# Performance work log

Hardware: AMD Instinct MI355X
Metric: run time of the kernel (lower is better)

## Reference

```python
import jax, jax.numpy as jnp
import numpy as np

A, V, T = 32, 32, 128          # per-modality hidden dims
PF = 128                       # post_fusion_dim
FUSED = (A + 1) * (V + 1) * (T + 1)  # 140481
B = 256


def setup_inputs() -> dict:
    key = jax.random.key(0)
    ks = jax.random.split(key, 9)
    s1 = 1.0 / np.sqrt(FUSED)
    s2 = 1.0 / np.sqrt(PF)
    return {
        "audio_x": jax.random.normal(ks[0], (B, A), dtype=jnp.float32),
        "video_x": jax.random.normal(ks[1], (B, V), dtype=jnp.float32),
        "text_x": jax.random.normal(ks[2], (B, T), dtype=jnp.float32),
        "W1": jax.random.uniform(ks[3], (FUSED, PF), jnp.float32, -s1, s1),
        "b1": jax.random.uniform(ks[4], (PF,), jnp.float32, -s1, s1),
        "W2": jax.random.uniform(ks[5], (PF, PF), jnp.float32, -s2, s2),
        "b2": jax.random.uniform(ks[6], (PF,), jnp.float32, -s2, s2),
        "W3": jax.random.uniform(ks[7], (PF, 1), jnp.float32, -s2, s2),
        "b3": jax.random.uniform(ks[8], (1,), jnp.float32, -s2, s2),
    }


def reference(audio_x, video_x, text_x, W1, b1, W2, b2, W3, b3):
    b = audio_x.shape[0]
    ones = jnp.ones((b, 1), dtype=audio_x.dtype)
    a = jnp.concatenate([ones, audio_x], axis=1)  # (B, A+1)
    v = jnp.concatenate([ones, video_x], axis=1)  # (B, V+1)
    t = jnp.concatenate([ones, text_x], axis=1)   # (B, T+1)
    # trilinear outer product, flattened: (B, (A+1)*(V+1)*(T+1))
    fusion = jnp.einsum("ba,bv,bt->bavt", a, v, t).reshape(b, -1)
    h1 = jax.nn.relu(fusion @ W1 + b1)
    h2 = jax.nn.relu(h1 @ W2 + b2)
    return h2 @ W3 + b3
```

## Files before the change

kernel.cpp:

```cpp
#include <hip/hip_runtime.h>
#include <hip/hip_bf16.h>
#include <stdint.h>

#define BATCH 256
#define PFD 128
#define T1 129
#define NPAIRS 1089
#define BK2 136
#define CHUNK 8

typedef short bf16x8 __attribute__((ext_vector_type(8)));
typedef float f32x4 __attribute__((ext_vector_type(4)));

static __device__ __forceinline__ float float_of(unsigned u){ union{float f;unsigned u;}x;x.u=u;return x.f; }
static __device__ __forceinline__ unsigned pk_bf16(float a, float b){
  union { __hip_bfloat162 h; unsigned u; } c;
  c.h = __float22bfloat162_rn(make_float2(a, b));
  return c.u;
}

__global__ __launch_bounds__(512, 2) void tfn_k1(
    const float* __restrict__ audio, const float* __restrict__ video,
    const float* __restrict__ text, const float* __restrict__ W1,
    unsigned short* __restrict__ part, int S) {
  __shared__ __align__(16) short b_lds[2][PFD * BK2];
  __shared__ __align__(16) float av_lds[BATCH * CHUNK];

  const int tid = threadIdx.x;
  const int bk = blockIdx.x;
  const int npb = NPAIRS / S, rem0 = NPAIRS % S;
  const int p0 = bk * npb + (bk < rem0 ? bk : rem0);
  const int np = npb + (bk < rem0 ? 1 : 0);

  const int wave = tid >> 6, lane = tid & 63;
  const int l15 = lane & 15, quad = lane >> 4;
  const int sn = tid & 127, skg = tid >> 7;

  float treg[2][32];
  float t128r[2];
  #pragma unroll
  for (int mt = 0; mt < 2; ++mt) {
    const int m = wave * 32 + mt * 16 + l15;
    t128r[mt] = text[m * 128 + 127];
    #pragma unroll
    for (int ks = 0; ks < 4; ++ks)
      #pragma unroll
      for (int j = 0; j < 8; ++j) {
        const int it = ks * 32 + quad * 8 + j;
        treg[mt][ks * 8 + j] = (it == 0) ? 1.0f : text[m * 128 + it - 1];
      }
  }

  f32x4 acc[2][8];
  #pragma unroll
  for (int a = 0; a < 2; ++a)
    #pragma unroll
    for (int b = 0; b < 8; ++b) acc[a][b] = f32x4{0.f, 0.f, 0.f, 0.f};

  float pf[32], rv[8];

  for (int c0 = 0; c0 < np; c0 += CHUNK) {
    const int nc = (np - c0) < CHUNK ? (np - c0) : CHUNK;
    const int pbase = p0 + c0;
    __syncthreads();
    if (tid < BATCH) {
      const int m = tid;
      for (int j = 0; j < nc; ++j) {
        int p = pbase + j;
        int ia = p / 33, iv = p - ia * 33;
        float a = (ia == 0) ? 1.0f : audio[m * 32 + ia - 1];
        float v = (iv == 0) ? 1.0f : video[m * 32 + iv - 1];
        av_lds[m * CHUNK + j] = a * v;
      }
    }
    #pragma unroll
    for (int j = 0; j < 8; ++j) {
      int kk = skg * 8 + j;
      rv[j] = (kk < nc) ? W1[((long)(pbase + kk) * T1 + 128) * PFD + sn] : 0.0f;
    }
    {
      const long rb = (long)pbase * T1;
      #pragma unroll
      for (int g = 0; g < 4; ++g)
        #pragma unroll
        for (int j = 0; j < 8; ++j)
          pf[g * 8 + j] = W1[(rb + g * 32 + skg * 8 + j) * PFD + sn];
    }
    for (int sp = 0; sp < nc; ++sp) {
      {
        union { bf16x8 v; unsigned u[4]; } w;
        #pragma unroll
        for (int g = 0; g < 4; ++g) {
          #pragma unroll
          for (int d = 0; d < 4; ++d)
            w.u[d] = pk_bf16(pf[g * 8 + 2 * d], pf[g * 8 + 2 * d + 1]);
          *(bf16x8*)&b_lds[sp & 1][sn * BK2 + g * 32 + skg * 8] = w.v;
        }
      }
      __syncthreads();
      if (sp + 1 < nc) {
        const long rb = (long)(pbase + sp + 1) * T1;
        #pragma unroll
        for (int g = 0; g < 4; ++g)
          #pragma unroll
          for (int j = 0; j < 8; ++j)
            pf[g * 8 + j] = W1[(rb + g * 32 + skg * 8 + j) * PFD + sn];
      }
      const float avm0 = av_lds[(wave * 32 + l15) * CHUNK + sp];
      const float avm1 = av_lds[(wave * 32 + 16 + l15) * CHUNK + sp];
      #pragma unroll
      for (int ks = 0; ks < 4; ++ks) {
        bf16x8 A0, A1;
        {
          union { bf16x8 v; unsigned u[4]; } c0u, c1u;
          #pragma unroll
          for (int d = 0; d < 4; ++d) {
            c0u.u[d] = pk_bf16(avm0 * treg[0][ks * 8 + 2 * d], avm0 * treg[0][ks * 8 + 2 * d + 1]);
            c1u.u[d] = pk_bf16(avm1 * treg[1][ks * 8 + 2 * d], avm1 * treg[1][ks * 8 + 2 * d + 1]);
          }
          A0 = c0u.v; A1 = c1u.v;
        }
        #pragma unroll
        for (int nt = 0; nt < 8; ++nt) {
          bf16x8 bf = *(const bf16x8*)&b_lds[sp & 1][(nt * 16 + l15) * BK2 + ks * 32 + quad * 8];
          acc[0][nt] = __builtin_amdgcn_mfma_f32_16x16x32_bf16(A0, bf, acc[0][nt], 0, 0, 0);
          acc[1][nt] = __builtin_amdgcn_mfma_f32_16x16x32_bf16(A1, bf, acc[1][nt], 0, 0, 0);
        }
      }
    }
    __syncthreads();
    {
      union { bf16x8 v; unsigned u[4]; } w;
      #pragma unroll
      for (int d = 0; d < 4; ++d) w.u[d] = pk_bf16(rv[2 * d], rv[2 * d + 1]);
      *(bf16x8*)&b_lds[0][sn * BK2 + skg * 8] = w.v;
    }
    __syncthreads();
    {
      bf16x8 A[2];
      #pragma unroll
      for (int mt = 0; mt < 2; ++mt) {
        const int m = wave * 32 + mt * 16 + l15;
        union { bf16x8 v; unsigned u[4]; } c;
        #pragma unroll
        for (int d = 0; d < 4; ++d) {
          int k0 = quad * 8 + 2 * d, k1 = k0 + 1;
          float f0 = (k0 < nc) ? av_lds[m * CHUNK + k0] * t128r[mt] : 0.0f;
          float f1 = (k1 < nc) ? av_lds[m * CHUNK + k1] * t128r[mt] : 0.0f;
          c.u[d] = pk_bf16(f0, f1);
        }
        A[mt] = c.v;
      }
      #pragma unroll
      for (int nt = 0; nt < 8; ++nt) {
        bf16x8 bf = *(const bf16x8*)&b_lds[0][(nt * 16 + l15) * BK2 + quad * 8];
        acc[0][nt] = __builtin_amdgcn_mfma_f32_16x16x32_bf16(A[0], bf, acc[0][nt], 0, 0, 0);
        acc[1][nt] = __builtin_amdgcn_mfma_f32_16x16x32_bf16(A[1], bf, acc[1][nt], 0, 0, 0);
      }
    }
  }

  #pragma unroll
  for (int mt = 0; mt < 2; ++mt)
    #pragma unroll
    for (int r = 0; r < 4; ++r) {
      const int m = wave * 32 + mt * 16 + quad * 4 + r;
      union { bf16x8 v; unsigned u[4]; } w;
      #pragma unroll
      for (int d = 0; d < 4; ++d) w.u[d] = pk_bf16(acc[mt][2 * d][r], acc[mt][2 * d + 1][r]);
      *(bf16x8*)&part[((size_t)m * S + bk) * PFD + l15 * 8] = w.v;
    }
}

__global__ __launch_bounds__(1024) void tfn_k2(
    const unsigned short* __restrict__ part, const float* __restrict__ b1,
    const float* __restrict__ W2, const float* __restrict__ b2,
    const float* __restrict__ W3, const float* __restrict__ b3,
    float* __restrict__ out, int S) {
  __shared__ float sred[1024 * 4];
  __shared__ float h1s[PFD];
  __shared__ float a2s[1024];
  __shared__ float red[2];
  const int m = blockIdx.x, tid = threadIdx.x;
  const int g = tid & 31, q = tid >> 5;
  const unsigned short* base = part + (size_t)m * S * PFD;
  float s0 = 0, s1 = 0, s2 = 0, s3 = 0;
  for (int bkk = q; bkk < S; bkk += 32) {
    uint2 v = *(const uint2*)&base[(size_t)bkk * PFD + g * 4];
    s0 += float_of(v.x << 16);
    s1 += float_of(v.x & 0xFFFF0000u);
    s2 += float_of(v.y << 16);
    s3 += float_of(v.y & 0xFFFF0000u);
  }
  sred[tid * 4 + 0] = s0; sred[tid * 4 + 1] = s1;
  sred[tid * 4 + 2] = s2; sred[tid * 4 + 3] = s3;
  __syncthreads();
  if (tid < PFD) {
    const int p = tid;
    float h = 0;
    #pragma unroll
    for (int bl = 0; bl < 32; ++bl) h += sred[(bl * 32 + (p >> 2)) * 4 + (p & 3)];
    const int n = (p & 7) * 16 + (p >> 3);
    h1s[n] = fmaxf(h + b1[n], 0.0f);
  }
  __syncthreads();
  const int n = tid & 127, kq = tid >> 7;
  float a2 = 0.0f;
  const int k0 = kq * 16;
  #pragma unroll
  for (int k = 0; k < 16; ++k) a2 += h1s[k0 + k] * W2[(k0 + k) * PFD + n];
  a2s[tid] = a2;
  __syncthreads();
  if (tid < 128) {
    float h2 = 0.0f;
    #pragma unroll
    for (int j = 0; j < 8; ++j) h2 += a2s[n + 128 * j];
    h2 = fmaxf(h2 + b2[n], 0.0f);
    float pr = h2 * W3[n];
    #pragma unroll
    for (int off = 32; off > 0; off >>= 1) pr += __shfl_down(pr, off);
    if ((tid & 63) == 0) red[tid >> 6] = pr;
  }
  __syncthreads();
  if (tid == 0) out[m] = red[0] + red[1] + b3[0];
}

extern "C" void kernel_launch(void* const* d_in, const int* in_sizes, int n_in,
                              void* d_out, int out_size, void* d_ws, size_t ws_size,
                              hipStream_t stream) {
  const float* audio = (const float*)d_in[0];
  const float* video = (const float*)d_in[1];
  const float* text  = (const float*)d_in[2];
  const float* W1 = (const float*)d_in[3];
  const float* b1 = (const float*)d_in[4];
  const float* W2 = (const float*)d_in[5];
  const float* b2 = (const float*)d_in[6];
  const float* W3 = (const float*)d_in[7];
  const float* b3 = (const float*)d_in[8];
  unsigned short* part = (unsigned short*)d_ws;

  const size_t slab = (size_t)BATCH * PFD * sizeof(unsigned short);
  int S = (int)(ws_size / slab);
  if (S > 256) S = 256;
  if (S < 1) S = 1;

  tfn_k1<<<S, 512, 0, stream>>>(audio, video, text, W1, part, S);
  tfn_k2<<<BATCH, 1024, 0, stream>>>(part, b1, W2, b2, W3, b3, (float*)d_out, S);
}
```

Baseline: 135.9 us.

## Double-buffer W1 register prefetch two pairs ahead with raw barriers

Splits the W1 register prefetch into two buffers so loads for a pair are issued two iterations before they are staged into LDS. It also replaces __syncthreads with an lgkmcnt wait plus s_barrier, so outstanding global loads no longer have to drain at each barrier. This is meant to hide global-memory latency behind the MFMA work. The cost is 32 more live registers, which may hurt occupancy at 512 threads with 2 blocks per CU or cause spills. Loads past the end are clamped to the last pair, so some reads are redundant.

```diff
diff --git a/kernel.cpp b/kernel.cpp
--- a/kernel.cpp
+++ b/kernel.cpp
@@ -57,7 +57,7 @@
     #pragma unroll
     for (int b = 0; b < 8; ++b) acc[a][b] = f32x4{0.f, 0.f, 0.f, 0.f};
 
-  float pf[32], rv[8];
+  float pfA[32], pfB[32], rv[8];
 
   for (int c0 = 0; c0 < np; c0 += CHUNK) {
     const int nc = (np - c0) < CHUNK ? (np - c0) : CHUNK;
@@ -78,34 +78,26 @@
       int kk = skg * 8 + j;
       rv[j] = (kk < nc) ? W1[((long)(pbase + kk) * T1 + 128) * PFD + sn] : 0.0f;
     }
-    {
-      const long rb = (long)pbase * T1;
+
+    auto load_pf = [&](float* pf, int pairIdx) {
+      const long rb = (long)(pbase + pairIdx) * T1;
       #pragma unroll
       for (int g = 0; g < 4; ++g)
         #pragma unroll
         for (int j = 0; j < 8; ++j)
           pf[g * 8 + j] = W1[(rb + g * 32 + skg * 8 + j) * PFD + sn];
-    }
-    for (int sp = 0; sp < nc; ++sp) {
-      {
-        union { bf16x8 v; unsigned u[4]; } w;
-        #pragma unroll
-        for (int g = 0; g < 4; ++g) {
-          #pragma unroll
-          for (int d = 0; d < 4; ++d)
-            w.u[d] = pk_bf16(pf[g * 8 + 2 * d], pf[g * 8 + 2 * d + 1]);
-          *(bf16x8*)&b_lds[sp & 1][sn * BK2 + g * 32 + skg * 8] = w.v;
-        }
-      }
-      __syncthreads();
-      if (sp + 1 < nc) {
-        const long rb = (long)(pbase + sp + 1) * T1;
-        #pragma unroll
-        for (int g = 0; g < 4; ++g)
-          #pragma unroll
-          for (int j = 0; j < 8; ++j)
-            pf[g * 8 + j] = W1[(rb + g * 32 + skg * 8 + j) * PFD + sn];
-      }
+    };
+    auto stage = [&](const float* pf, int buf) {
+      union { bf16x8 v; unsigned u[4]; } w;
+      #pragma unroll
+      for (int g = 0; g < 4; ++g) {
+        #pragma unroll
+        for (int d = 0; d < 4; ++d)
+          w.u[d] = pk_bf16(pf[g * 8 + 2 * d], pf[g * 8 + 2 * d + 1]);
+        *(bf16x8*)&b_lds[buf][sn * BK2 + g * 32 + skg * 8] = w.v;
+      }
+    };
+    auto compute = [&](int sp, int buf) {
       const float avm0 = av_lds[(wave * 32 + l15) * CHUNK + sp];
       const float avm1 = av_lds[(wave * 32 + 16 + l15) * CHUNK + sp];
       #pragma unroll
@@ -122,12 +114,32 @@
         }
         #pragma unroll
         for (int nt = 0; nt < 8; ++nt) {
-          bf16x8 bf = *(const bf16x8*)&b_lds[sp & 1][(nt * 16 + l15) * BK2 + ks * 32 + quad * 8];
+          bf16x8 bf = *(const bf16x8*)&b_lds[buf][(nt * 16 + l15) * BK2 + ks * 32 + quad * 8];
           acc[0][nt] = __builtin_amdgcn_mfma_f32_16x16x32_bf16(A0, bf, acc[0][nt], 0, 0, 0);
           acc[1][nt] = __builtin_amdgcn_mfma_f32_16x16x32_bf16(A1, bf, acc[1][nt], 0, 0, 0);
         }
       }
-    }
+    };
+
+    load_pf(pfA, 0);
+    load_pf(pfB, nc > 1 ? 1 : 0);
+
+    for (int sp = 0; sp < nc; sp += 2) {
+      stage(pfA, 0);
+      { int nx = sp + 2 < nc ? sp + 2 : nc - 1; load_pf(pfA, nx); }
+      asm volatile("s_waitcnt lgkmcnt(0)" ::: "memory");
+      __builtin_amdgcn_s_barrier();
+      asm volatile("" ::: "memory");
+      compute(sp, 0);
+      if (sp + 1 >= nc) break;
+      stage(pfB, 1);
+      { int nx = sp + 3 < nc ? sp + 3 : nc - 1; load_pf(pfB, nx); }
+      asm volatile("s_waitcnt lgkmcnt(0)" ::: "memory");
+      __builtin_amdgcn_s_barrier();
+      asm volatile("" ::: "memory");
+      compute(sp + 1, 1);
+    }
+
     __syncthreads();
     {
       union { bf16x8 v; unsigned u[4]; } w;
```

After: 144.6 us. 1.06x slower.

## Stage W1 slices into LDS with async global_load_lds instead of register prefetch

Applied to the files above, without the earlier changes.

Each next W1 slice (128x128 fp32) is now copied straight into a new fp32 LDS staging buffer with 16-byte global_load_lds transfers, replacing the 32-register prefetch array. Threads then read the fp32 values from LDS, convert them to bf16 and write the single-buffered B tile. The aim is to cut register pressure and let the weight stream overlap compute without holding data in VGPRs. In exchange LDS use grows to roughly 107KB per block, which limits occupancy to one block per CU, the B tile loses its double buffer and gains an extra barrier, and correctness relies on the async LDS writes being waited on before the reads.

```diff
diff --git a/kernel.cpp b/kernel.cpp
--- a/kernel.cpp
+++ b/kernel.cpp
@@ -19,11 +19,19 @@
   return c.u;
 }
 
+static __device__ __forceinline__ void gl_lds16(const float* g, float* l) {
+  __builtin_amdgcn_global_load_lds(
+      (const __attribute__((address_space(1))) unsigned int*)g,
+      (__attribute__((address_space(3))) unsigned int*)l,
+      16, 0, 0);
+}
+
 __global__ __launch_bounds__(512, 2) void tfn_k1(
     const float* __restrict__ audio, const float* __restrict__ video,
     const float* __restrict__ text, const float* __restrict__ W1,
     unsigned short* __restrict__ part, int S) {
-  __shared__ __align__(16) short b_lds[2][PFD * BK2];
+  __shared__ __align__(16) float w_lds[128 * 128];
+  __shared__ __align__(16) short b_lds[PFD * BK2];
   __shared__ __align__(16) float av_lds[BATCH * CHUNK];
 
   const int tid = threadIdx.x;
@@ -57,7 +65,7 @@
     #pragma unroll
     for (int b = 0; b < 8; ++b) acc[a][b] = f32x4{0.f, 0.f, 0.f, 0.f};
 
-  float pf[32], rv[8];
+  float rv[8];
 
   for (int c0 = 0; c0 < np; c0 += CHUNK) {
     const int nc = (np - c0) < CHUNK ? (np - c0) : CHUNK;
@@ -79,32 +87,34 @@
       rv[j] = (kk < nc) ? W1[((long)(pbase + kk) * T1 + 128) * PFD + sn] : 0.0f;
     }
     {
-      const long rb = (long)pbase * T1;
-      #pragma unroll
-      for (int g = 0; g < 4; ++g)
-        #pragma unroll
-        for (int j = 0; j < 8; ++j)
-          pf[g * 8 + j] = W1[(rb + g * 32 + skg * 8 + j) * PFD + sn];
+      const float* gsrc = W1 + (long)pbase * (T1 * PFD);
+      #pragma unroll
+      for (int g = 0; g < 8; ++g)
+        gl_lds16(gsrc + g * 2048 + wave * 256 + lane * 4,
+                 &w_lds[g * 2048 + wave * 256]);
     }
     for (int sp = 0; sp < nc; ++sp) {
+      __syncthreads();
       {
         union { bf16x8 v; unsigned u[4]; } w;
         #pragma unroll
         for (int g = 0; g < 4; ++g) {
+          float f[8];
           #pragma unroll
-          for (int d = 0; d < 4; ++d)
-            w.u[d] = pk_bf16(pf[g * 8 + 2 * d], pf[g * 8 + 2 * d + 1]);
-          *(bf16x8*)&b_lds[sp & 1][sn * BK2 + g * 32 + skg * 8] = w.v;
+          for (int j = 0; j < 8; ++j)
+            f[j] = w_lds[(g * 32 + skg * 8 + j) * 128 + sn];
+          #pragma unroll
+          for (int d = 0; d < 4; ++d) w.u[d] = pk_bf16(f[2 * d], f[2 * d + 1]);
+          *(bf16x8*)&b_lds[sn * BK2 + g * 32 + skg * 8] = w.v;
         }
       }
       __syncthreads();
       if (sp + 1 < nc) {
-        const long rb = (long)(pbase + sp + 1) * T1;
-        #pragma unroll
-        for (int g = 0; g < 4; ++g)
-          #pragma unroll
-          for (int j = 0; j < 8; ++j)
-            pf[g * 8 + j] = W1[(rb + g * 32 + skg * 8 + j) * PFD + sn];
+        const float* gsrc = W1 + (long)(pbase + sp + 1) * (T1 * PFD);
+        #pragma unroll
+        for (int g = 0; g < 8; ++g)
+          gl_lds16(gsrc + g * 2048 + wave * 256 + lane * 4,
+                   &w_lds[g * 2048 + wave * 256]);
       }
       const float avm0 = av_lds[(wave * 32 + l15) * CHUNK + sp];
       const float avm1 = av_lds[(wave * 32 + 16 + l15) * CHUNK + sp];
@@ -122,7 +132,7 @@
         }
         #pragma unroll
         for (int nt = 0; nt < 8; ++nt) {
-          bf16x8 bf = *(const bf16x8*)&b_lds[sp & 1][(nt * 16 + l15) * BK2 + ks * 32 + quad * 8];
+          bf16x8 bf = *(const bf16x8*)&b_lds[(nt * 16 + l15) * BK2 + ks * 32 + quad * 8];
           acc[0][nt] = __builtin_amdgcn_mfma_f32_16x16x32_bf16(A0, bf, acc[0][nt], 0, 0, 0);
           acc[1][nt] = __builtin_amdgcn_mfma_f32_16x16x32_bf16(A1, bf, acc[1][nt], 0, 0, 0);
         }
@@ -133,7 +143,7 @@
       union { bf16x8 v; unsigned u[4]; } w;
       #pragma unroll
       for (int d = 0; d < 4; ++d) w.u[d] = pk_bf16(rv[2 * d], rv[2 * d + 1]);
-      *(bf16x8*)&b_lds[0][sn * BK2 + skg * 8] = w.v;
+      *(bf16x8*)&b_lds[sn * BK2 + skg * 8] = w.v;
     }
     __syncthreads();
     {
@@ -153,7 +163,7 @@
       }
       #pragma unroll
       for (int nt = 0; nt < 8; ++nt) {
-        bf16x8 bf = *(const bf16x8*)&b_lds[0][(nt * 16 + l15) * BK2 + quad * 8];
+        bf16x8 bf = *(const bf16x8*)&b_lds[(nt * 16 + l15) * BK2 + quad * 8];
         acc[0][nt] = __builtin_amdgcn_mfma_f32_16x16x32_bf16(A[0], bf, acc[0][nt], 0, 0, 0);
         acc[1][nt] = __builtin_amdgcn_mfma_f32_16x16x32_bf16(A[1], bf, acc[1][nt], 0, 0, 0);
       }
```

Result: no change. 137.2 us (+0.9%).

## Split batch across two half-size blocks and halve the W1 K-slab per step

Applied to the files above, without the earlier changes.

The first kernel now launches twice as many blocks, each with 256 threads covering one half of the batch (128 rows) for the same slice of (audio, video) pairs. The per-step W1 staging tile is halved to 64 rows, with the loop doing two sub-steps per pair, so LDS use per block drops. The intent is more resident blocks and better latency hiding on the many CUs. The cost is that every W1 slice is now loaded and converted by two blocks, doubling global and L2 weight traffic.

```diff
diff --git a/kernel.cpp b/kernel.cpp
--- a/kernel.cpp
+++ b/kernel.cpp
@@ -6,7 +6,7 @@
 #define PFD 128
 #define T1 129
 #define NPAIRS 1089
-#define BK2 136
+#define BH 72
 #define CHUNK 8
 
 typedef short bf16x8 __attribute__((ext_vector_type(8)));
@@ -19,18 +19,20 @@
   return c.u;
 }
 
-__global__ __launch_bounds__(512, 2) void tfn_k1(
+__global__ __launch_bounds__(256, 2) void tfn_k1(
     const float* __restrict__ audio, const float* __restrict__ video,
     const float* __restrict__ text, const float* __restrict__ W1,
     unsigned short* __restrict__ part, int S) {
-  __shared__ __align__(16) short b_lds[2][PFD * BK2];
-  __shared__ __align__(16) float av_lds[BATCH * CHUNK];
+  __shared__ __align__(16) short b_lds[2][PFD * BH];
+  __shared__ __align__(16) float av_lds[128 * CHUNK];
 
   const int tid = threadIdx.x;
   const int bk = blockIdx.x;
+  const int sidx = bk % S;
+  const int mh = bk / S;
   const int npb = NPAIRS / S, rem0 = NPAIRS % S;
-  const int p0 = bk * npb + (bk < rem0 ? bk : rem0);
-  const int np = npb + (bk < rem0 ? 1 : 0);
+  const int p0 = sidx * npb + (sidx < rem0 ? sidx : rem0);
+  const int np = npb + (sidx < rem0 ? 1 : 0);
 
   const int wave = tid >> 6, lane = tid & 63;
   const int l15 = lane & 15, quad = lane >> 4;
@@ -40,7 +42,7 @@
   float t128r[2];
   #pragma unroll
   for (int mt = 0; mt < 2; ++mt) {
-    const int m = wave * 32 + mt * 16 + l15;
+    const int m = mh * 128 + wave * 32 + mt * 16 + l15;
     t128r[mt] = text[m * 128 + 127];
     #pragma unroll
     for (int ks = 0; ks < 4; ++ks)
@@ -63,14 +65,15 @@
     const int nc = (np - c0) < CHUNK ? (np - c0) : CHUNK;
     const int pbase = p0 + c0;
     __syncthreads();
-    if (tid < BATCH) {
-      const int m = tid;
+    if (tid < 128) {
+      const int ml = tid;
+      const int m = mh * 128 + ml;
       for (int j = 0; j < nc; ++j) {
         int p = pbase + j;
         int ia = p / 33, iv = p - ia * 33;
         float a = (ia == 0) ? 1.0f : audio[m * 32 + ia - 1];
         float v = (iv == 0) ? 1.0f : video[m * 32 + iv - 1];
-        av_lds[m * CHUNK + j] = a * v;
+        av_lds[ml * CHUNK + j] = a * v;
       }
     }
     #pragma unroll
@@ -78,15 +81,21 @@
       int kk = skg * 8 + j;
       rv[j] = (kk < nc) ? W1[((long)(pbase + kk) * T1 + 128) * PFD + sn] : 0.0f;
     }
-    {
-      const long rb = (long)pbase * T1;
+
+    auto load_pf = [&](int s) {
+      const long rb = (long)(pbase + (s >> 1)) * T1 + (s & 1) * 64;
       #pragma unroll
       for (int g = 0; g < 4; ++g)
         #pragma unroll
         for (int j = 0; j < 8; ++j)
-          pf[g * 8 + j] = W1[(rb + g * 32 + skg * 8 + j) * PFD + sn];
-    }
-    for (int sp = 0; sp < nc; ++sp) {
+          pf[g * 8 + j] = W1[(rb + g * 16 + skg * 8 + j) * PFD + sn];
+    };
+
+    load_pf(0);
+
+    const int NS = 2 * nc;
+    for (int s = 0; s < NS; ++s) {
+      const int buf = s & 1;
       {
         union { bf16x8 v; unsigned u[4]; } w;
         #pragma unroll
@@ -94,66 +103,64 @@
           #pragma unroll
           for (int d = 0; d < 4; ++d)
             w.u[d] = pk_bf16(pf[g * 8 + 2 * d], pf[g * 8 + 2 * d + 1]);
-          *(bf16x8*)&b_lds[sp & 1][sn * BK2 + g * 32 + skg * 8] = w.v;
+          *(bf16x8*)&b_lds[buf][sn * BH + g * 16 + skg * 8] = w.v;
         }
       }
       __syncthreads();
-      if (sp + 1 < nc) {
-        const long rb = (long)(pbase + sp + 1) * T1;
-        #pragma unroll
-        for (int g = 0; g < 4; ++g)
+      if (s + 1 < NS) load_pf(s + 1);
+      {
+        const int sp = s >> 1, h = s & 1;
+        const float avm0 = av_lds[(wave * 32 + l15) * CHUNK + sp];
+        const float avm1 = av_lds[(wave * 32 + 16 + l15) * CHUNK + sp];
+        #pragma unroll
+        for (int ksl = 0; ksl < 2; ++ksl) {
+          const int ks = h * 2 + ksl;
+          bf16x8 A0, A1;
+          {
+            union { bf16x8 v; unsigned u[4]; } c0u, c1u;
+            #pragma unroll
+            for (int d = 0; d < 4; ++d) {
+              c0u.u[d] = pk_bf16(avm0 * treg[0][ks * 8 + 2 * d], avm0 * treg[0][ks * 8 + 2 * d + 1]);
+              c1u.u[d] = pk_bf16(avm1 * treg[1][ks * 8 + 2 * d], avm1 * treg[1][ks * 8 + 2 * d + 1]);
+            }
+            A0 = c0u.v; A1 = c1u.v;
+          }
           #pragma unroll
-          for (int j = 0; j < 8; ++j)
-            pf[g * 8 + j] = W1[(rb + g * 32 + skg * 8 + j) * PFD + sn];
-      }
-      const float avm0 = av_lds[(wave * 32 + l15) * CHUNK + sp];
-      const float avm1 = av_lds[(wave * 32 + 16 + l15) * CHUNK + sp];
-      #pragma unroll
-      for (int ks = 0; ks < 4; ++ks) {
-        bf16x8 A0, A1;
-        {
-          union { bf16x8 v; unsigned u[4]; } c0u, c1u;
-          #pragma unroll
-          for (int d = 0; d < 4; ++d) {
-            c0u.u[d] = pk_bf16(avm0 * treg[0][ks * 8 + 2 * d], avm0 * treg[0][ks * 8 + 2 * d + 1]);
-            c1u.u[d] = pk_bf16(avm1 * treg[1][ks * 8 + 2 * d], avm1 * treg[1][ks * 8 + 2 * d + 1]);
+          for (int nt = 0; nt < 8; ++nt) {
+            bf16x8 bf = *(const bf16x8*)&b_lds[buf][(nt * 16 + l15) * BH + ksl * 32 + quad * 8];
+            acc[0][nt] = __builtin_amdgcn_mfma_f32_16x16x32_bf16(A0, bf, acc[0][nt], 0, 0, 0);
+            acc[1][nt] = __builtin_amdgcn_mfma_f32_16x16x32_bf16(A1, bf, acc[1][nt], 0, 0, 0);
           }
-          A0 = c0u.v; A1 = c1u.v;
         }
-        #pragma unroll
-        for (int nt = 0; nt < 8; ++nt) {
-          bf16x8 bf = *(const bf16x8*)&b_lds[sp & 1][(nt * 16 + l15) * BK2 + ks * 32 + quad * 8];
-          acc[0][nt] = __builtin_amdgcn_mfma_f32_16x16x32_bf16(A0, bf, acc[0][nt], 0, 0, 0);
-          acc[1][nt] = __builtin_amdgcn_mfma_f32_16x16x32_bf16(A1, bf, acc[1][nt], 0, 0, 0);
-        }
-      }
-    }
+      }
+    }
+
     __syncthreads();
     {
       union { bf16x8 v; unsigned u[4]; } w;
       #pragma unroll
       for (int d = 0; d < 4; ++d) w.u[d] = pk_bf16(rv[2 * d], rv[2 * d + 1]);
-      *(bf16x8*)&b_lds[0][sn * BK2 + skg * 8] = w.v;
+      *(bf16x8*)&b_lds[0][sn * BH + skg * 8] = w.v;
     }
     __syncthreads();
     {
       bf16x8 A[2];
       #pragma unroll
       for (int mt = 0; mt < 2; ++mt) {
-        const int m = wave * 32 + mt * 16 + l15;
+        const int ml = wave * 32 + mt * 16 + l15;
         union { bf16x8 v; unsigned u[4]; } c;
         #pragma unroll
         for (int d = 0; d < 4; ++d) {
           int k0 = quad * 8 + 2 * d, k1 = k0 + 1;
-          float f0 = (k0 < nc) ? av_lds[m * CHUNK + k0] * t128r[mt] : 0.0f;
-          float f1 = (k1 < nc) ? av_lds[m * CHUNK + k1] * t128r[mt] : 0.0f;
+          float f0 = (k0 < nc) ? av_lds[ml * CHUNK + k0] * t128r[mt] : 0.0f;
+          float f1 = (k1 < nc) ? av_lds[ml * CHUNK + k1] * t128r[mt] : 0.0f;
           c.u[d] = pk_bf16(f0, f1);
         }
         A[mt] = c.v;
       }
       #pragma unroll
       for (int nt = 0; nt < 8; ++nt) {
-        bf16x8 bf = *(const bf16x8*)&b_lds[0][(nt * 16 + l15) * BK2 + quad * 8];
+        bf16x8 bf = *(const bf16x8*)&b_lds[0][(nt * 16 + l15) * BH + quad * 8];
         acc[0][nt] = __builtin_amdgcn_mfma_f32_16x16x32_bf16(A[0], bf, acc[0][nt], 0, 0, 0);
         acc[1][nt] = __builtin_amdgcn_mfma_f32_16x16x32_bf16(A[1], bf, acc[1][nt], 0, 0, 0);
       }
@@ -164,11 +171,11 @@
   for (int mt = 0; mt < 2; ++mt)
     #pragma unroll
     for (int r = 0; r < 4; ++r) {
-      const int m = wave * 32 + mt * 16 + quad * 4 + r;
+      const int m = mh * 128 + wave * 32 + mt * 16 + quad * 4 + r;
       union { bf16x8 v; unsigned u[4]; } w;
       #pragma unroll
       for (int d = 0; d < 4; ++d) w.u[d] = pk_bf16(acc[mt][2 * d][r], acc[mt][2 * d + 1][r]);
-      *(bf16x8*)&part[((size_t)m * S + bk) * PFD + l15 * 8] = w.v;
+      *(bf16x8*)&part[((size_t)m * S + sidx) * PFD + l15 * 8] = w.v;
     }
 }
 
@@ -244,6 +251,6 @@
   if (S > 256) S = 256;
   if (S < 1) S = 1;
 
-  tfn_k1<<<S, 512, 0, stream>>>(audio, video, text, W1, part, S);
+  tfn_k1<<<2 * S, 256, 0, stream>>>(audio, video, text, W1, part, S);
   tfn_k2<<<BATCH, 1024, 0, stream>>>(part, b1, W2, b2, W3, b3, (float*)d_out, S);
 }
```

Result: slower. 175.2 us (+28.9%).
